# Performance work log

Hardware: AMD Instinct MI355X
Metric: run time of the kernel (lower is better)

The kernel has to match this reference:

```python
import jax, jax.numpy as jnp
import numpy as np

B, N, D = 4, 4096, 512
E = 4 * D            # expanded_dim = 2048
TAIL = E // 2        # tail_dim = 1024
HALF = TAIL // 2     # mt_half = 512
HEAD = E - TAIL      # head_dim = 1024
EPS_RMS = 1e-6
EPS_NORM = 1e-12


def setup_inputs() -> dict:
    key = jax.random.key(0)
    k = jax.random.split(key, 6)
    x = jax.random.normal(k[0], (B, N, D), dtype=jnp.float32)
    g = jnp.ones((D,), dtype=jnp.float32)                                   # RMSNorm gain
    W1 = jax.random.normal(k[1], (D, E), dtype=jnp.float32) * 0.02          # Enricher linear
    b1 = jnp.zeros((E,), dtype=jnp.float32)
    V = jax.random.normal(k[2], (N, N), dtype=jnp.float32) * 0.02           # learned positional matrix slice
    bias = jnp.zeros((HALF,), dtype=jnp.float32)                            # contextualizer bias
    Wf = jax.random.normal(k[3], (HEAD + HALF, D), dtype=jnp.float32) * 0.02  # Fuser linear (no bias)
    return {"x": x, "g": g, "W1": W1, "b1": b1, "V": V, "bias": bias, "Wf": Wf}


def reference(x, g, W1, b1, V, bias, Wf):
    # RMSNorm
    xn = x * jax.lax.rsqrt(jnp.mean(jnp.square(x), axis=-1, keepdims=True) + EPS_RMS) * g
    # Enricher: relu(linear)^2
    enriched = jnp.square(jax.nn.relu(xn @ W1 + b1))                        # [B, N, E]
    head = enriched[..., :HEAD]                                             # [B, N, HEAD]
    tail = enriched[..., HEAD:]                                             # [B, N, TAIL]
    # Contextualizer
    x_left = tail[..., :HALF]
    x_right = tail[..., HALF:]
    nrm = jnp.sqrt(jnp.sum(jnp.square(x_right), axis=-1, keepdims=True))
    xr_n = x_right / jnp.maximum(nrm, EPS_NORM)                             # F.normalize, p=2
    cos = jnp.einsum('bnd,bmd->bnm', xr_n, xr_n)                            # [B, N, N] cosine sim
    weighted = V[None, :, :] * cos                                          # elementwise learned V
    ctx = jnp.einsum('bnm,bmd->bnd', weighted, xr_n)                        # chunked-path bmm uses x_right_norm
    ctx = jax.nn.sigmoid(ctx + bias)
    gated = x_left * ctx                                                    # [B, N, HALF]
    # Fuser + residual
    out = jnp.concatenate([head, gated], axis=-1) @ Wf                      # [B, N, D]
    return x + out
```

## Files before the change

### kernel.cpp

```cpp
#include <hip/hip_runtime.h>
#include <stdint.h>

typedef unsigned short u16;
typedef unsigned long long u64;
typedef __attribute__((ext_vector_type(8))) short bf16x8;
typedef __attribute__((ext_vector_type(4))) float f32x4;
typedef __attribute__((ext_vector_type(16))) float f32x16;
typedef __attribute__((ext_vector_type(4))) unsigned int u32x4;
typedef __attribute__((ext_vector_type(4))) unsigned short u16x4;

#define DEV static __device__ __forceinline__

DEV u16 f2bf(float f){
  unsigned u = __builtin_bit_cast(unsigned, f);
  u += 0x7fffu + ((u >> 16) & 1u);
  return (u16)(u >> 16);
}
DEV float bf2f(u16 v){
  unsigned u = ((unsigned)v) << 16;
  return __builtin_bit_cast(float, u);
}

DEV void async_lds16(const void* g, void* l){
  __builtin_amdgcn_global_load_lds(
      (const __attribute__((address_space(1))) unsigned int*)g,
      (__attribute__((address_space(3))) unsigned int*)l, 16, 0, 0);
}

DEV f32x4 mfma16(bf16x8 a, bf16x8 b, f32x4 c){
  return __builtin_amdgcn_mfma_f32_16x16x32_bf16(a, b, c, 0, 0, 0);
}
DEV f32x16 mfma32(bf16x8 a, bf16x8 b, f32x16 c){
  return __builtin_amdgcn_mfma_f32_32x32x16_bf16(a, b, c, 0, 0, 0);
}

__global__ __launch_bounds__(64) void k_rms(const float* __restrict__ x,
                                            const float* __restrict__ g,
                                            u16* __restrict__ xn){
  const int row = blockIdx.x;
  const int l = threadIdx.x;
  const float* xr = x + (size_t)row * 512 + l * 8;
  f32x4 a = *(const f32x4*)xr;
  f32x4 c = *(const f32x4*)(xr + 4);
  float s = a[0]*a[0]+a[1]*a[1]+a[2]*a[2]+a[3]*a[3]
          + c[0]*c[0]+c[1]*c[1]+c[2]*c[2]+c[3]*c[3];
  #pragma unroll
  for (int off = 32; off >= 1; off >>= 1) s += __shfl_xor(s, off);
  float sc = rsqrtf(s * (1.f/512.f) + 1e-6f);
  f32x4 g0 = *(const f32x4*)&g[l*8];
  f32x4 g1 = *(const f32x4*)&g[l*8+4];
  u32x4 o;
  o[0] = (unsigned)f2bf(a[0]*sc*g0[0]) | ((unsigned)f2bf(a[1]*sc*g0[1]) << 16);
  o[1] = (unsigned)f2bf(a[2]*sc*g0[2]) | ((unsigned)f2bf(a[3]*sc*g0[3]) << 16);
  o[2] = (unsigned)f2bf(c[0]*sc*g1[0]) | ((unsigned)f2bf(c[1]*sc*g1[1]) << 16);
  o[3] = (unsigned)f2bf(c[2]*sc*g1[2]) | ((unsigned)f2bf(c[3]*sc*g1[3]) << 16);
  *(u32x4*)&xn[(size_t)row*512 + l*8] = o;
}

__global__ __launch_bounds__(64) void k_norm(const float* __restrict__ xr_in,
                                             u16* __restrict__ xrn){
  const int row = blockIdx.x;
  const int l = threadIdx.x;
  const float* xr = xr_in + (size_t)row * 512 + l * 8;
  f32x4 a = *(const f32x4*)xr;
  f32x4 c = *(const f32x4*)(xr + 4);
  float s = a[0]*a[0]+a[1]*a[1]+a[2]*a[2]+a[3]*a[3]
          + c[0]*c[0]+c[1]*c[1]+c[2]*c[2]+c[3]*c[3];
  #pragma unroll
  for (int off = 32; off >= 1; off >>= 1) s += __shfl_xor(s, off);
  float sc = 1.f / fmaxf(sqrtf(s), 1e-12f);
  u32x4 o;
  o[0] = (unsigned)f2bf(a[0]*sc) | ((unsigned)f2bf(a[1]*sc) << 16);
  o[1] = (unsigned)f2bf(a[2]*sc) | ((unsigned)f2bf(a[3]*sc) << 16);
  o[2] = (unsigned)f2bf(c[0]*sc) | ((unsigned)f2bf(c[1]*sc) << 16);
  o[3] = (unsigned)f2bf(c[2]*sc) | ((unsigned)f2bf(c[3]*sc) << 16);
  *(u32x4*)&xrn[(size_t)row*512 + l*8] = o;
}

__global__ __launch_bounds__(256) void k_tr32(const float* __restrict__ in,
                                              u16* __restrict__ out, int R, int C){
  __shared__ float tile[32][33];
  const int t = threadIdx.x;
  const int r = t >> 3;
  const int c4 = (t & 7) << 2;
  const int r0 = blockIdx.y << 5, c0 = blockIdx.x << 5;
  f32x4 v = *(const f32x4*)&in[(size_t)(r0 + r) * C + c0 + c4];
  tile[r][c4+0]=v[0]; tile[r][c4+1]=v[1]; tile[r][c4+2]=v[2]; tile[r][c4+3]=v[3];
  __syncthreads();
  u64 o =
      (u64)f2bf(tile[c4+0][r])
    | ((u64)f2bf(tile[c4+1][r]) << 16)
    | ((u64)f2bf(tile[c4+2][r]) << 32)
    | ((u64)f2bf(tile[c4+3][r]) << 48);
  *(u64*)&out[(size_t)(c0 + r) * R + r0 + c4] = o;
}

__global__ __launch_bounds__(256) void k_trb(const u16* __restrict__ in,
                                             u16* __restrict__ out, int R, int C){
  __shared__ u16 tile[32][40];
  const int t = threadIdx.x;
  const int r = t >> 3;
  const int c4 = (t & 7) << 2;
  const size_t bb = (size_t)blockIdx.z * R * C;
  const int r0 = blockIdx.y << 5, c0 = blockIdx.x << 5;
  u64 v = *(const u64*)&in[bb + (size_t)(r0 + r)*C + c0 + c4];
  tile[r][c4+0]=(u16)v; tile[r][c4+1]=(u16)(v>>16);
  tile[r][c4+2]=(u16)(v>>32); tile[r][c4+3]=(u16)(v>>48);
  __syncthreads();
  u64 o =
      (u64)tile[c4+0][r]
    | ((u64)tile[c4+1][r] << 16)
    | ((u64)tile[c4+2][r] << 32)
    | ((u64)tile[c4+3][r] << 48);
  *(u64*)&out[bb + (size_t)(c0 + r) * R + r0 + c4] = o;
}

__global__ __launch_bounds__(256) void k_gemm1(const u16* __restrict__ A,
                                               const u16* __restrict__ Bt,
                                               const float* __restrict__ b1,
                                               u16* __restrict__ head,
                                               float* __restrict__ xleft,
                                               float* __restrict__ xright){
  __shared__ u16 As[2][128*32];
  __shared__ u16 Bs[2][128*32];
  const int t = threadIdx.x;
  const int l = t & 63;
  const int w = t >> 6;
  const int wr = w >> 1, wc = w & 1;
  const int m0 = blockIdx.x << 7;
  const int n0 = blockIdx.y << 7;
  const int ra = t >> 2;
  const int kb = (t & 3) << 3;
  const int lr = l & 15, lh = l >> 4;
  f32x4 acc[4][4];
  #pragma unroll
  for (int i=0;i<4;i++)
    #pragma unroll
    for (int j=0;j<4;j++)
      #pragma unroll
      for (int r=0;r<4;r++) acc[i][j][r] = 0.f;

  async_lds16(A  + (size_t)(m0 + ra)*512      + kb, &As[0][t*8]);
  async_lds16(A  + (size_t)(m0 + 64 + ra)*512 + kb, &As[0][2048 + t*8]);
  async_lds16(Bt + (size_t)(n0 + ra)*512      + kb, &Bs[0][t*8]);
  async_lds16(Bt + (size_t)(n0 + 64 + ra)*512 + kb, &Bs[0][2048 + t*8]);
  __syncthreads();

  int cur = 0;
  for (int k0 = 0; k0 < 512; k0 += 32){
    if (k0 + 32 < 512){
      const int kn = k0 + 32;
      const int nb = cur ^ 1;
      async_lds16(A  + (size_t)(m0 + ra)*512      + kn + kb, &As[nb][t*8]);
      async_lds16(A  + (size_t)(m0 + 64 + ra)*512 + kn + kb, &As[nb][2048 + t*8]);
      async_lds16(Bt + (size_t)(n0 + ra)*512      + kn + kb, &Bs[nb][t*8]);
      async_lds16(Bt + (size_t)(n0 + 64 + ra)*512 + kn + kb, &Bs[nb][2048 + t*8]);
    }
    bf16x8 af[4], bfr[4];
    #pragma unroll
    for (int i=0;i<4;i++){
      af[i]  = *(const bf16x8*)&As[cur][(wr*64 + i*16 + lr)*32 + lh*8];
      bfr[i] = *(const bf16x8*)&Bs[cur][(wc*64 + i*16 + lr)*32 + lh*8];
    }
    #pragma unroll
    for (int i=0;i<4;i++)
      #pragma unroll
      for (int j=0;j<4;j++)
        acc[i][j] = mfma16(af[i], bfr[j], acc[i][j]);
    __syncthreads();
    cur ^= 1;
  }
  #pragma unroll
  for (int i=0;i<4;i++){
    #pragma unroll
    for (int j=0;j<4;j++){
      int c = n0 + wc*64 + j*16 + lr;
      float bb = b1[c];
      #pragma unroll
      for (int r=0;r<4;r++){
        int m = m0 + wr*64 + i*16 + lh*4 + r;
        float v = acc[i][j][r] + bb;
        v = v > 0.f ? v*v : 0.f;
        if (c < 1024)      head[(size_t)m*1024 + c] = f2bf(v);
        else if (c < 1536) xleft[(size_t)m*512 + (c - 1024)] = v;
        else               xright[(size_t)m*512 + (c - 1536)] = v;
      }
    }
  }
}

__global__ __launch_bounds__(256) void k_gemm3(const u16* __restrict__ head,
                                               const u16* __restrict__ gated,
                                               const u16* __restrict__ Wft,
                                               const float* __restrict__ x,
                                               float* __restrict__ out){
  __shared__ u16 As[2][128*32];
  __shared__ u16 Bs[2][128*32];
  const int t = threadIdx.x;
  const int l = t & 63;
  const int w = t >> 6;
  const int wr = w >> 1, wc = w & 1;
  const int m0 = blockIdx.x << 7;
  const int n0 = blockIdx.y << 7;
  const int ra = t >> 2;
  const int kb = (t & 3) << 3;
  const int lr = l & 15, lh = l >> 4;
  f32x4 acc[4][4];
  #pragma unroll
  for (int i=0;i<4;i++)
    #pragma unroll
    for (int j=0;j<4;j++)
      #pragma unroll
      for (int r=0;r<4;r++) acc[i][j][r] = 0.f;

  auto stage = [&](int nb, int k0){
    const u16* sa; size_t lda; int kk;
    if (k0 < 1024){ sa = head;  lda = 1024; kk = k0; }
    else          { sa = gated; lda = 512;  kk = k0 - 1024; }
    async_lds16(sa + (size_t)(m0 + ra)*lda      + kk + kb, &As[nb][t*8]);
    async_lds16(sa + (size_t)(m0 + 64 + ra)*lda + kk + kb, &As[nb][2048 + t*8]);
    async_lds16(Wft + (size_t)(n0 + ra)*1536      + k0 + kb, &Bs[nb][t*8]);
    async_lds16(Wft + (size_t)(n0 + 64 + ra)*1536 + k0 + kb, &Bs[nb][2048 + t*8]);
  };
  stage(0, 0);
  __syncthreads();

  int cur = 0;
  for (int k0 = 0; k0 < 1536; k0 += 32){
    if (k0 + 32 < 1536) stage(cur ^ 1, k0 + 32);
    bf16x8 af[4], bfr[4];
    #pragma unroll
    for (int i=0;i<4;i++){
      af[i]  = *(const bf16x8*)&As[cur][(wr*64 + i*16 + lr)*32 + lh*8];
      bfr[i] = *(const bf16x8*)&Bs[cur][(wc*64 + i*16 + lr)*32 + lh*8];
    }
    #pragma unroll
    for (int i=0;i<4;i++)
      #pragma unroll
      for (int j=0;j<4;j++)
        acc[i][j] = mfma16(af[i], bfr[j], acc[i][j]);
    __syncthreads();
    cur ^= 1;
  }
  #pragma unroll
  for (int i=0;i<4;i++){
    #pragma unroll
    for (int j=0;j<4;j++){
      int c = n0 + wc*64 + j*16 + lr;
      #pragma unroll
      for (int r=0;r<4;r++){
        int m = m0 + wr*64 + i*16 + lh*4 + r;
        size_t gi = (size_t)m*512 + c;
        out[gi] = x[gi] + acc[i][j][r];
      }
    }
  }
}

__global__ __launch_bounds__(512, 2) void k_attn(const u16* __restrict__ xrn,
                                                 const u16* __restrict__ xrT,
                                                 const float* __restrict__ V,
                                                 const float* __restrict__ bias,
                                                 const float* __restrict__ xleft,
                                                 u16* __restrict__ gated){
  __shared__ char smem[154624];
  char* km = smem;
  char* tt = smem + 65536;
  char* ps = smem + 131072;
  char* pb = smem + 149504;
  const int t = threadIdx.x;
  const int l = t & 63, w = t >> 6;
  const int wr = w >> 2, ks = w & 3, wc = (w >> 1) & 1, kq2 = w & 1;
  const int lo = l & 31, hi = l >> 5;
  const int bid = blockIdx.x;
  const int b  = (bid & 7) >> 1;
  const int n0 = ((((bid >> 3) << 1) | (bid & 1))) << 6;
  const u16* xb  = xrn + (size_t)b * (4096*512);
  const u16* xTb = xrT + (size_t)b * (512*4096);

  bf16x8 areg[8];
  {
    const u16* apt = xb + (size_t)(n0 + wr*32 + lo)*512 + ks*128 + hi*8;
    #pragma unroll
    for (int kq = 0; kq < 8; ++kq) areg[kq] = *(const bf16x8*)(apt + kq*16);
  }
  f32x16 acc[8];
  #pragma unroll
  for (int i = 0; i < 8; ++i)
    #pragma unroll
    for (int j = 0; j < 16; ++j) acc[i][j] = 0.f;

  const int prf = t >> 3;
  const int pc4 = (t & 7) << 2;
  const int wrr = prf >> 5, prr = prf & 31;

  #pragma unroll
  for (int c = 0; c < 4; ++c){
    int off = (c*512 + t)*16;
    int row = off >> 10, colb = off & 1023;
    async_lds16(xb + (size_t)row*512 + ((colb ^ ((row&7)<<4)) >> 1), km + off);
    int dr = off >> 6, cb2 = off & 63;
    async_lds16(xTb + (size_t)dr*4096 + ((cb2 ^ ((dr&6)<<3)) >> 1), tt + off);
  }
  __syncthreads();

  int cur = 0;
  for (int it = 0; it < 128; ++it){
    const int m0 = it << 5;
    f32x4 vf = *(const f32x4*)&V[(size_t)(n0 + prf)*4096 + m0 + pc4];
    if (it < 127){
      const int m1 = m0 + 32;
      const int nb = (cur ^ 1) * 32768;
      #pragma unroll
      for (int c = 0; c < 4; ++c){
        int off = (c*512 + t)*16;
        int row = off >> 10, colb = off & 1023;
        async_lds16(xb + (size_t)(m1 + row)*512 + ((colb ^ ((row&7)<<4)) >> 1),
                    km + nb + off);
        int dr = off >> 6, cb2 = off & 63;
        async_lds16(xTb + (size_t)dr*4096 + m1 + ((cb2 ^ ((dr&6)<<3)) >> 1),
                    tt + nb + off);
      }
    }
    f32x16 S0, S1;
    #pragma unroll
    for (int j = 0; j < 16; ++j){ S0[j] = 0.f; S1[j] = 0.f; }
    {
      const char* kbp = km + cur*32768 + lo*1024;
      const int swk = (lo & 7) << 4;
      #pragma unroll
      for (int kq = 0; kq < 8; kq += 2){
        bf16x8 b0 = *(const bf16x8*)(kbp + ((ks*256 + kq*32 + hi*16) ^ swk));
        bf16x8 b1 = *(const bf16x8*)(kbp + ((ks*256 + (kq+1)*32 + hi*16) ^ swk));
        S0 = mfma32(areg[kq],   b0, S0);
        S1 = mfma32(areg[kq+1], b1, S1);
      }
    }
    {
      char* pw = ps + ((wr*4 + ks)*32)*72 + lo*2;
      #pragma unroll
      for (int rg = 0; rg < 16; ++rg){
        int prow = (rg & 3) + 8*(rg >> 2) + 4*hi;
        *(u16*)(pw + prow*72) = f2bf(S0[rg] + S1[rg]);
      }
    }
    asm volatile("s_waitcnt lgkmcnt(0)" ::: "memory");
    __builtin_amdgcn_s_barrier();
    __builtin_amdgcn_sched_barrier(0);
    {
      float s0=0.f, s1=0.f, s2=0.f, s3=0.f;
      #pragma unroll
      for (int k2 = 0; k2 < 4; ++k2){
        u16x4 pv = *(const u16x4*)(ps + (((wrr*4 + k2)*32 + prr)*36 + pc4)*2);
        s0 += bf2f(pv[0]); s1 += bf2f(pv[1]); s2 += bf2f(pv[2]); s3 += bf2f(pv[3]);
      }
      u64 po = (u64)f2bf(s0 * vf[0])
             | ((u64)f2bf(s1 * vf[1]) << 16)
             | ((u64)f2bf(s2 * vf[2]) << 32)
             | ((u64)f2bf(s3 * vf[3]) << 48);
      *(u64*)(pb + (prf*40 + pc4)*2) = po;
    }
    asm volatile("s_waitcnt lgkmcnt(0)" ::: "memory");
    __builtin_amdgcn_s_barrier();
    __builtin_amdgcn_sched_barrier(0);
    {
      bf16x8 pa = *(const bf16x8*)(pb + (wr*32 + lo)*80 + kq2*32 + hi*16);
      const char* tb = tt + cur*32768;
      #pragma unroll
      for (int ds = 0; ds < 8; ++ds){
        int drow = wc*256 + ds*32 + lo;
        bf16x8 bfr = *(const bf16x8*)(tb + drow*64 +
                       ((kq2*32 + hi*16) ^ ((drow & 6) << 3)));
        acc[ds] = mfma32(pa, bfr, acc[ds]);
      }
    }
    __syncthreads();
    cur ^= 1;
  }

  float* red = (float*)smem;
  const int rbase = (wr*2 + wc) * 8192;
  if (kq2 == 1){
    #pragma unroll
    for (int ds = 0; ds < 8; ++ds)
      #pragma unroll
      for (int rg = 0; rg < 16; ++rg)
        red[rbase + (ds*16 + rg)*64 + l] = acc[ds][rg];
  }
  __syncthreads();
  if (kq2 == 0){
    #pragma unroll
    for (int ds = 0; ds < 8; ++ds){
      const int d = wc*256 + ds*32 + lo;
      const float bs = bias[d];
      #pragma unroll
      for (int rg = 0; rg < 16; ++rg){
        int row = n0 + wr*32 + (rg & 3) + 8*(rg >> 2) + 4*hi;
        float v = acc[ds][rg] + red[rbase + (ds*16 + rg)*64 + l] + bs;
        v = 1.f / (1.f + __expf(-v));
        size_t gi = (size_t)(b*4096 + row)*512 + d;
        gated[gi] = f2bf(xleft[gi] * v);
      }
    }
  }
}

extern "C" void kernel_launch(void* const* d_in, const int* in_sizes, int n_in,
                              void* d_out, int out_size, void* d_ws, size_t ws_size,
                              hipStream_t stream){
  const float* x    = (const float*)d_in[0];
  const float* g    = (const float*)d_in[1];
  const float* W1   = (const float*)d_in[2];
  const float* b1   = (const float*)d_in[3];
  const float* V    = (const float*)d_in[4];
  const float* bias = (const float*)d_in[5];
  const float* Wf   = (const float*)d_in[6];
  float* out = (float*)d_out;

  char* ws = (char*)d_ws;
  const size_t MB = 1024u*1024u;
  u16*   xn     = (u16*)  (ws + 0*MB);
  u16*   W1t    = (u16*)  (ws + 16*MB);
  u16*   Wft    = (u16*)  (ws + 18*MB);
  u16*   head   = (u16*)  (ws + 20*MB);
  float* xleft  = (float*)(ws + 52*MB);
  float* xright = (float*)(ws + 84*MB);
  u16*   gated  = (u16*)  (ws + 84*MB);
  u16*   xrn    = (u16*)  (ws + 116*MB);
  u16*   xrT    = (u16*)  (ws + 132*MB);

  k_rms  <<<dim3(16384),      dim3(64),  0, stream>>>(x, g, xn);
  k_tr32 <<<dim3(64, 16),     dim3(256), 0, stream>>>(W1, W1t, 512, 2048);
  k_tr32 <<<dim3(16, 48),     dim3(256), 0, stream>>>(Wf, Wft, 1536, 512);
  k_gemm1<<<dim3(128, 16),    dim3(256), 0, stream>>>(xn, W1t, b1, head, xleft, xright);
  k_norm <<<dim3(16384),      dim3(64),  0, stream>>>(xright, xrn);
  k_trb  <<<dim3(16, 128, 4), dim3(256), 0, stream>>>(xrn, xrT, 4096, 512);
  k_attn <<<dim3(256),        dim3(512), 0, stream>>>(xrn, xrT, V, bias, xleft, gated);
  k_gemm3<<<dim3(128, 4),     dim3(256), 0, stream>>>(head, gated, Wft, x, out);
}
```

Before: 385.0 us.

## Warp-specialize attention kernel into S-producer and PV-consumer wave groups

Splits the eight waves into four that compute the cosine-similarity tile S and four that apply V and accumulate P·X, with the consumer lagging one iteration behind through a double-buffered S tile in LDS. This removes one barrier per iteration and the final cross-wave reduction of the accumulators, since each consumer wave now covers the full K range of its tile. The cost is a deeper software pipeline, extra LDS, twice the A-fragment registers in producer waves, and possible imbalance between the two wave groups.

```diff
diff --git a/kernel.cpp b/kernel.cpp
--- a/kernel.cpp
+++ b/kernel.cpp
@@ -20,6 +20,7 @@
   unsigned u = ((unsigned)v) << 16;
   return __builtin_bit_cast(float, u);
 }
+DEV float bitf(unsigned u){ return __builtin_bit_cast(float, u); }
 
 DEV void async_lds16(const void* g, void* l){
   __builtin_amdgcn_global_load_lds(
@@ -263,140 +264,142 @@
                                                  const float* __restrict__ bias,
                                                  const float* __restrict__ xleft,
                                                  u16* __restrict__ gated){
-  __shared__ char smem[154624];
+  __shared__ char smem[156672];
   char* km = smem;
   char* tt = smem + 65536;
   char* ps = smem + 131072;
-  char* pb = smem + 149504;
+  char* pb = smem + 151552;
   const int t = threadIdx.x;
   const int l = t & 63, w = t >> 6;
-  const int wr = w >> 2, ks = w & 3, wc = (w >> 1) & 1, kq2 = w & 1;
   const int lo = l & 31, hi = l >> 5;
+  const bool isS = (w < 4);
+  const int wr  = (w >> 1) & 1;
+  const int sub = w & 1;
   const int bid = blockIdx.x;
   const int b  = (bid & 7) >> 1;
   const int n0 = ((((bid >> 3) << 1) | (bid & 1))) << 6;
   const u16* xb  = xrn + (size_t)b * (4096*512);
   const u16* xTb = xrT + (size_t)b * (512*4096);
 
-  bf16x8 areg[8];
-  {
-    const u16* apt = xb + (size_t)(n0 + wr*32 + lo)*512 + ks*128 + hi*8;
-    #pragma unroll
-    for (int kq = 0; kq < 8; ++kq) areg[kq] = *(const bf16x8*)(apt + kq*16);
+  bf16x8 areg[16];
+  if (isS){
+    const u16* apt = xb + (size_t)(n0 + wr*32 + lo)*512 + sub*256 + hi*8;
+    #pragma unroll
+    for (int kq = 0; kq < 16; ++kq) areg[kq] = *(const bf16x8*)(apt + kq*16);
   }
   f32x16 acc[8];
   #pragma unroll
   for (int i = 0; i < 8; ++i)
     #pragma unroll
     for (int j = 0; j < 16; ++j) acc[i][j] = 0.f;
-
-  const int prf = t >> 3;
-  const int pc4 = (t & 7) << 2;
-  const int wrr = prf >> 5, prr = prf & 31;
 
   #pragma unroll
   for (int c = 0; c < 4; ++c){
     int off = (c*512 + t)*16;
     int row = off >> 10, colb = off & 1023;
     async_lds16(xb + (size_t)row*512 + ((colb ^ ((row&7)<<4)) >> 1), km + off);
-    int dr = off >> 6, cb2 = off & 63;
-    async_lds16(xTb + (size_t)dr*4096 + ((cb2 ^ ((dr&6)<<3)) >> 1), tt + off);
-  }
-  __syncthreads();
-
-  int cur = 0;
-  for (int it = 0; it < 128; ++it){
-    const int m0 = it << 5;
-    f32x4 vf = *(const f32x4*)&V[(size_t)(n0 + prf)*4096 + m0 + pc4];
+  }
+
+  f32x4 v0n = {0,0,0,0}, v1n = {0,0,0,0}, v0c = {0,0,0,0}, v1c = {0,0,0,0};
+
+  for (int it = 0; it <= 128; ++it){
+    __syncthreads();
     if (it < 127){
-      const int m1 = m0 + 32;
-      const int nb = (cur ^ 1) * 32768;
+      const int m1 = (it + 1) << 5;
+      const int nb = ((it + 1) & 1) * 32768;
       #pragma unroll
       for (int c = 0; c < 4; ++c){
         int off = (c*512 + t)*16;
         int row = off >> 10, colb = off & 1023;
         async_lds16(xb + (size_t)(m1 + row)*512 + ((colb ^ ((row&7)<<4)) >> 1),
                     km + nb + off);
+      }
+    }
+    if (it < 128){
+      const int mt = it << 5;
+      const int nb = (it & 1) * 32768;
+      #pragma unroll
+      for (int c = 0; c < 4; ++c){
+        int off = (c*512 + t)*16;
         int dr = off >> 6, cb2 = off & 63;
-        async_lds16(xTb + (size_t)dr*4096 + m1 + ((cb2 ^ ((dr&6)<<3)) >> 1),
+        async_lds16(xTb + (size_t)dr*4096 + mt + ((cb2 ^ ((dr&6)<<3)) >> 1),
                     tt + nb + off);
       }
     }
-    f32x16 S0, S1;
-    #pragma unroll
-    for (int j = 0; j < 16; ++j){ S0[j] = 0.f; S1[j] = 0.f; }
-    {
-      const char* kbp = km + cur*32768 + lo*1024;
-      const int swk = (lo & 7) << 4;
-      #pragma unroll
-      for (int kq = 0; kq < 8; kq += 2){
-        bf16x8 b0 = *(const bf16x8*)(kbp + ((ks*256 + kq*32 + hi*16) ^ swk));
-        bf16x8 b1 = *(const bf16x8*)(kbp + ((ks*256 + (kq+1)*32 + hi*16) ^ swk));
-        S0 = mfma32(areg[kq],   b0, S0);
-        S1 = mfma32(areg[kq+1], b1, S1);
-      }
-    }
-    {
-      char* pw = ps + ((wr*4 + ks)*32)*72 + lo*2;
-      #pragma unroll
-      for (int rg = 0; rg < 16; ++rg){
-        int prow = (rg & 3) + 8*(rg >> 2) + 4*hi;
-        *(u16*)(pw + prow*72) = f2bf(S0[rg] + S1[rg]);
+    if (isS){
+      if (it < 128){
+        f32x16 S0, S1;
+        #pragma unroll
+        for (int j = 0; j < 16; ++j){ S0[j] = 0.f; S1[j] = 0.f; }
+        const char* kbp = km + (it & 1)*32768 + lo*1024;
+        const int swk = (lo & 7) << 4;
+        #pragma unroll
+        for (int kq = 0; kq < 16; kq += 2){
+          bf16x8 b0 = *(const bf16x8*)(kbp + ((sub*512 + kq*32 + hi*16) ^ swk));
+          bf16x8 b1 = *(const bf16x8*)(kbp + ((sub*512 + (kq+1)*32 + hi*16) ^ swk));
+          S0 = mfma32(areg[kq],   b0, S0);
+          S1 = mfma32(areg[kq+1], b1, S1);
+        }
+        char* pw = ps + (it & 1)*10240 + (wr*2 + sub)*2560 + lo*2;
+        #pragma unroll
+        for (int rg = 0; rg < 16; ++rg){
+          int prow = (rg & 3) + 8*(rg >> 2) + 4*hi;
+          *(u16*)(pw + prow*80) = f2bf(S0[rg] + S1[rg]);
+        }
+      }
+    } else {
+      if (it < 128){
+        const float* vp = V + (size_t)(n0 + wr*32 + lo)*4096 + (it << 5)
+                        + sub*16 + hi*8;
+        v0n = *(const f32x4*)vp;
+        v1n = *(const f32x4*)(vp + 4);
+      }
+      if (it > 0){
+        const char* pr = ps + ((it - 1) & 1)*10240 + (wr*2)*2560 + lo*80
+                       + sub*32 + hi*16;
+        u32x4 qa = *(const u32x4*)pr;
+        u32x4 qb = *(const u32x4*)(pr + 2560);
+        u32x4 pk;
+        #pragma unroll
+        for (int e = 0; e < 4; ++e){
+          float se = bitf(qa[e] << 16) + bitf(qb[e] << 16);
+          float so = bitf(qa[e] & 0xffff0000u) + bitf(qb[e] & 0xffff0000u);
+          float ve = (e < 2) ? v0c[e*2]     : v1c[(e - 2)*2];
+          float vo = (e < 2) ? v0c[e*2 + 1] : v1c[(e - 2)*2 + 1];
+          pk[e] = (unsigned)f2bf(se * ve) | ((unsigned)f2bf(so * vo) << 16);
+        }
+        *(u32x4*)(pb + (wr*32 + lo)*80 + sub*32 + hi*16) = pk;
       }
     }
     asm volatile("s_waitcnt lgkmcnt(0)" ::: "memory");
     __builtin_amdgcn_s_barrier();
     __builtin_amdgcn_sched_barrier(0);
-    {
-      float s0=0.f, s1=0.f, s2=0.f, s3=0.f;
-      #pragma unroll
-      for (int k2 = 0; k2 < 4; ++k2){
-        u16x4 pv = *(const u16x4*)(ps + (((wrr*4 + k2)*32 + prr)*36 + pc4)*2);
-        s0 += bf2f(pv[0]); s1 += bf2f(pv[1]); s2 += bf2f(pv[2]); s3 += bf2f(pv[3]);
-      }
-      u64 po = (u64)f2bf(s0 * vf[0])
-             | ((u64)f2bf(s1 * vf[1]) << 16)
-             | ((u64)f2bf(s2 * vf[2]) << 32)
-             | ((u64)f2bf(s3 * vf[3]) << 48);
-      *(u64*)(pb + (prf*40 + pc4)*2) = po;
-    }
-    asm volatile("s_waitcnt lgkmcnt(0)" ::: "memory");
-    __builtin_amdgcn_s_barrier();
-    __builtin_amdgcn_sched_barrier(0);
-    {
-      bf16x8 pa = *(const bf16x8*)(pb + (wr*32 + lo)*80 + kq2*32 + hi*16);
-      const char* tb = tt + cur*32768;
-      #pragma unroll
-      for (int ds = 0; ds < 8; ++ds){
-        int drow = wc*256 + ds*32 + lo;
-        bf16x8 bfr = *(const bf16x8*)(tb + drow*64 +
-                       ((kq2*32 + hi*16) ^ ((drow & 6) << 3)));
-        acc[ds] = mfma32(pa, bfr, acc[ds]);
-      }
-    }
-    __syncthreads();
-    cur ^= 1;
-  }
-
-  float* red = (float*)smem;
-  const int rbase = (wr*2 + wc) * 8192;
-  if (kq2 == 1){
-    #pragma unroll
-    for (int ds = 0; ds < 8; ++ds)
-      #pragma unroll
-      for (int rg = 0; rg < 16; ++rg)
-        red[rbase + (ds*16 + rg)*64 + l] = acc[ds][rg];
-  }
-  __syncthreads();
-  if (kq2 == 0){
+    if (!isS && it > 0){
+      const char* tb = tt + ((it - 1) & 1)*32768;
+      #pragma unroll
+      for (int kq2 = 0; kq2 < 2; ++kq2){
+        bf16x8 pa = *(const bf16x8*)(pb + (wr*32 + lo)*80 + kq2*32 + hi*16);
+        #pragma unroll
+        for (int ds = 0; ds < 8; ++ds){
+          int drow = sub*256 + ds*32 + lo;
+          bf16x8 bfr = *(const bf16x8*)(tb + drow*64 +
+                         ((kq2*32 + hi*16) ^ ((drow & 6) << 3)));
+          acc[ds] = mfma32(pa, bfr, acc[ds]);
+        }
+      }
+    }
+    v0c = v0n; v1c = v1n;
+  }
+
+  if (!isS){
     #pragma unroll
     for (int ds = 0; ds < 8; ++ds){
-      const int d = wc*256 + ds*32 + lo;
+      const int d = sub*256 + ds*32 + lo;
       const float bs = bias[d];
       #pragma unroll
       for (int rg = 0; rg < 16; ++rg){
         int row = n0 + wr*32 + (rg & 3) + 8*(rg >> 2) + 4*hi;
-        float v = acc[ds][rg] + red[rbase + (ds*16 + rg)*64 + l] + bs;
+        float v = acc[ds][rg] + bs;
         v = 1.f / (1.f + __expf(-v));
         size_t gi = (size_t)(b*4096 + row)*512 + d;
         gated[gi] = f2bf(xleft[gi] * v);
```

After: 679.2 us. 1.76x slower.

## Split fused attention kernel into separate S-GEMM and PV-GEMM with materialized P

Applied to the files above, without the earlier changes.

Replaces the fused cosine-attention kernel with two plain tiled GEMM kernels: one computes the cosine matrix times V and writes a bf16 P matrix to global memory, the other multiplies P by the transposed normalized keys and applies the sigmoid gate. The workspace layout is reorganized so all batches' P fit when the workspace is large enough, with a per-batch loop as fallback. This trades the fused kernel's LDS round-trips and barriers for simpler, higher-occupancy GEMMs at the cost of writing and reading a 32 MB-per-batch intermediate.

```diff
diff --git a/kernel.cpp b/kernel.cpp
--- a/kernel.cpp
+++ b/kernel.cpp
@@ -5,9 +5,7 @@
 typedef unsigned long long u64;
 typedef __attribute__((ext_vector_type(8))) short bf16x8;
 typedef __attribute__((ext_vector_type(4))) float f32x4;
-typedef __attribute__((ext_vector_type(16))) float f32x16;
 typedef __attribute__((ext_vector_type(4))) unsigned int u32x4;
-typedef __attribute__((ext_vector_type(4))) unsigned short u16x4;
 
 #define DEV static __device__ __forceinline__
 
@@ -16,10 +14,6 @@
   u += 0x7fffu + ((u >> 16) & 1u);
   return (u16)(u >> 16);
 }
-DEV float bf2f(u16 v){
-  unsigned u = ((unsigned)v) << 16;
-  return __builtin_bit_cast(float, u);
-}
 
 DEV void async_lds16(const void* g, void* l){
   __builtin_amdgcn_global_load_lds(
@@ -29,9 +23,6 @@
 
 DEV f32x4 mfma16(bf16x8 a, bf16x8 b, f32x4 c){
   return __builtin_amdgcn_mfma_f32_16x16x32_bf16(a, b, c, 0, 0, 0);
-}
-DEV f32x16 mfma32(bf16x8 a, bf16x8 b, f32x16 c){
-  return __builtin_amdgcn_mfma_f32_32x32x16_bf16(a, b, c, 0, 0, 0);
 }
 
 __global__ __launch_bounds__(64) void k_rms(const float* __restrict__ x,
@@ -257,148 +248,143 @@
   }
 }
 
-__global__ __launch_bounds__(512, 2) void k_attn(const u16* __restrict__ xrn,
-                                                 const u16* __restrict__ xrT,
-                                                 const float* __restrict__ V,
-                                                 const float* __restrict__ bias,
-                                                 const float* __restrict__ xleft,
-                                                 u16* __restrict__ gated){
-  __shared__ char smem[154624];
-  char* km = smem;
-  char* tt = smem + 65536;
-  char* ps = smem + 131072;
-  char* pb = smem + 149504;
-  const int t = threadIdx.x;
-  const int l = t & 63, w = t >> 6;
-  const int wr = w >> 2, ks = w & 3, wc = (w >> 1) & 1, kq2 = w & 1;
-  const int lo = l & 31, hi = l >> 5;
-  const int bid = blockIdx.x;
-  const int b  = (bid & 7) >> 1;
-  const int n0 = ((((bid >> 3) << 1) | (bid & 1))) << 6;
-  const u16* xb  = xrn + (size_t)b * (4096*512);
-  const u16* xTb = xrT + (size_t)b * (512*4096);
-
-  bf16x8 areg[8];
-  {
-    const u16* apt = xb + (size_t)(n0 + wr*32 + lo)*512 + ks*128 + hi*8;
-    #pragma unroll
-    for (int kq = 0; kq < 8; ++kq) areg[kq] = *(const bf16x8*)(apt + kq*16);
-  }
-  f32x16 acc[8];
-  #pragma unroll
-  for (int i = 0; i < 8; ++i)
-    #pragma unroll
-    for (int j = 0; j < 16; ++j) acc[i][j] = 0.f;
-
-  const int prf = t >> 3;
-  const int pc4 = (t & 7) << 2;
-  const int wrr = prf >> 5, prr = prf & 31;
-
-  #pragma unroll
-  for (int c = 0; c < 4; ++c){
-    int off = (c*512 + t)*16;
-    int row = off >> 10, colb = off & 1023;
-    async_lds16(xb + (size_t)row*512 + ((colb ^ ((row&7)<<4)) >> 1), km + off);
-    int dr = off >> 6, cb2 = off & 63;
-    async_lds16(xTb + (size_t)dr*4096 + ((cb2 ^ ((dr&6)<<3)) >> 1), tt + off);
-  }
+__global__ __launch_bounds__(256) void k_sgemm(const u16* __restrict__ xrn,
+                                               const float* __restrict__ V,
+                                               u16* __restrict__ P,
+                                               size_t pstride, int b0){
+  __shared__ u16 As[2][128*32];
+  __shared__ u16 Bs[2][128*32];
+  const int t = threadIdx.x;
+  const int l = t & 63;
+  const int w = t >> 6;
+  const int wr = w >> 1, wc = w & 1;
+  const int m0 = blockIdx.x << 7;
+  const int n0 = blockIdx.y << 7;
+  const int b  = b0 + blockIdx.z;
+  const u16* xb = xrn + (size_t)b * (4096*512);
+  u16* Pb = P + (size_t)blockIdx.z * pstride;
+  const int ra = t >> 2;
+  const int kb = (t & 3) << 3;
+  const int lr = l & 15, lh = l >> 4;
+  f32x4 acc[4][4];
+  #pragma unroll
+  for (int i=0;i<4;i++)
+    #pragma unroll
+    for (int j=0;j<4;j++)
+      #pragma unroll
+      for (int r=0;r<4;r++) acc[i][j][r] = 0.f;
+
+  async_lds16(xb + (size_t)(n0 + ra)*512      + kb, &As[0][t*8]);
+  async_lds16(xb + (size_t)(n0 + 64 + ra)*512 + kb, &As[0][2048 + t*8]);
+  async_lds16(xb + (size_t)(m0 + ra)*512      + kb, &Bs[0][t*8]);
+  async_lds16(xb + (size_t)(m0 + 64 + ra)*512 + kb, &Bs[0][2048 + t*8]);
   __syncthreads();
 
   int cur = 0;
-  for (int it = 0; it < 128; ++it){
-    const int m0 = it << 5;
-    f32x4 vf = *(const f32x4*)&V[(size_t)(n0 + prf)*4096 + m0 + pc4];
-    if (it < 127){
-      const int m1 = m0 + 32;
-      const int nb = (cur ^ 1) * 32768;
-      #pragma unroll
-      for (int c = 0; c < 4; ++c){
-        int off = (c*512 + t)*16;
-        int row = off >> 10, colb = off & 1023;
-        async_lds16(xb + (size_t)(m1 + row)*512 + ((colb ^ ((row&7)<<4)) >> 1),
-                    km + nb + off);
-        int dr = off >> 6, cb2 = off & 63;
-        async_lds16(xTb + (size_t)dr*4096 + m1 + ((cb2 ^ ((dr&6)<<3)) >> 1),
-                    tt + nb + off);
-      }
-    }
-    f32x16 S0, S1;
-    #pragma unroll
-    for (int j = 0; j < 16; ++j){ S0[j] = 0.f; S1[j] = 0.f; }
-    {
-      const char* kbp = km + cur*32768 + lo*1024;
-      const int swk = (lo & 7) << 4;
-      #pragma unroll
-      for (int kq = 0; kq < 8; kq += 2){
-        bf16x8 b0 = *(const bf16x8*)(kbp + ((ks*256 + kq*32 + hi*16) ^ swk));
-        bf16x8 b1 = *(const bf16x8*)(kbp + ((ks*256 + (kq+1)*32 + hi*16) ^ swk));
-        S0 = mfma32(areg[kq],   b0, S0);
-        S1 = mfma32(areg[kq+1], b1, S1);
-      }
-    }
-    {
-      char* pw = ps + ((wr*4 + ks)*32)*72 + lo*2;
-      #pragma unroll
-      for (int rg = 0; rg < 16; ++rg){
-        int prow = (rg & 3) + 8*(rg >> 2) + 4*hi;
-        *(u16*)(pw + prow*72) = f2bf(S0[rg] + S1[rg]);
-      }
-    }
-    asm volatile("s_waitcnt lgkmcnt(0)" ::: "memory");
-    __builtin_amdgcn_s_barrier();
-    __builtin_amdgcn_sched_barrier(0);
-    {
-      float s0=0.f, s1=0.f, s2=0.f, s3=0.f;
-      #pragma unroll
-      for (int k2 = 0; k2 < 4; ++k2){
-        u16x4 pv = *(const u16x4*)(ps + (((wrr*4 + k2)*32 + prr)*36 + pc4)*2);
-        s0 += bf2f(pv[0]); s1 += bf2f(pv[1]); s2 += bf2f(pv[2]); s3 += bf2f(pv[3]);
-      }
-      u64 po = (u64)f2bf(s0 * vf[0])
-             | ((u64)f2bf(s1 * vf[1]) << 16)
-             | ((u64)f2bf(s2 * vf[2]) << 32)
-             | ((u64)f2bf(s3 * vf[3]) << 48);
-      *(u64*)(pb + (prf*40 + pc4)*2) = po;
-    }
-    asm volatile("s_waitcnt lgkmcnt(0)" ::: "memory");
-    __builtin_amdgcn_s_barrier();
-    __builtin_amdgcn_sched_barrier(0);
-    {
-      bf16x8 pa = *(const bf16x8*)(pb + (wr*32 + lo)*80 + kq2*32 + hi*16);
-      const char* tb = tt + cur*32768;
-      #pragma unroll
-      for (int ds = 0; ds < 8; ++ds){
-        int drow = wc*256 + ds*32 + lo;
-        bf16x8 bfr = *(const bf16x8*)(tb + drow*64 +
-                       ((kq2*32 + hi*16) ^ ((drow & 6) << 3)));
-        acc[ds] = mfma32(pa, bfr, acc[ds]);
-      }
-    }
+  for (int k0 = 0; k0 < 512; k0 += 32){
+    if (k0 + 32 < 512){
+      const int kn = k0 + 32;
+      const int nb = cur ^ 1;
+      async_lds16(xb + (size_t)(n0 + ra)*512      + kn + kb, &As[nb][t*8]);
+      async_lds16(xb + (size_t)(n0 + 64 + ra)*512 + kn + kb, &As[nb][2048 + t*8]);
+      async_lds16(xb + (size_t)(m0 + ra)*512      + kn + kb, &Bs[nb][t*8]);
+      async_lds16(xb + (size_t)(m0 + 64 + ra)*512 + kn + kb, &Bs[nb][2048 + t*8]);
+    }
+    bf16x8 af[4], bfr[4];
+    #pragma unroll
+    for (int i=0;i<4;i++){
+      af[i]  = *(const bf16x8*)&As[cur][(wr*64 + i*16 + lr)*32 + lh*8];
+      bfr[i] = *(const bf16x8*)&Bs[cur][(wc*64 + i*16 + lr)*32 + lh*8];
+    }
+    #pragma unroll
+    for (int i=0;i<4;i++)
+      #pragma unroll
+      for (int j=0;j<4;j++)
+        acc[i][j] = mfma16(af[i], bfr[j], acc[i][j]);
     __syncthreads();
     cur ^= 1;
   }
-
-  float* red = (float*)smem;
-  const int rbase = (wr*2 + wc) * 8192;
-  if (kq2 == 1){
-    #pragma unroll
-    for (int ds = 0; ds < 8; ++ds)
-      #pragma unroll
-      for (int rg = 0; rg < 16; ++rg)
-        red[rbase + (ds*16 + rg)*64 + l] = acc[ds][rg];
-  }
-  __syncthreads();
-  if (kq2 == 0){
-    #pragma unroll
-    for (int ds = 0; ds < 8; ++ds){
-      const int d = wc*256 + ds*32 + lo;
-      const float bs = bias[d];
-      #pragma unroll
-      for (int rg = 0; rg < 16; ++rg){
-        int row = n0 + wr*32 + (rg & 3) + 8*(rg >> 2) + 4*hi;
-        float v = acc[ds][rg] + red[rbase + (ds*16 + rg)*64 + l] + bs;
+  #pragma unroll
+  for (int i=0;i<4;i++){
+    #pragma unroll
+    for (int j=0;j<4;j++){
+      int col = m0 + wc*64 + j*16 + lr;
+      #pragma unroll
+      for (int r=0;r<4;r++){
+        int row = n0 + wr*64 + i*16 + lh*4 + r;
+        float vv = V[(size_t)row*4096 + col];
+        Pb[(size_t)row*4096 + col] = f2bf(acc[i][j][r] * vv);
+      }
+    }
+  }
+}
+
+__global__ __launch_bounds__(256) void k_pvgemm(const u16* __restrict__ P,
+                                                size_t pstride,
+                                                const u16* __restrict__ xrT,
+                                                const float* __restrict__ xleft,
+                                                const float* __restrict__ bias,
+                                                u16* __restrict__ gated, int b0){
+  __shared__ u16 As[2][64*32];
+  __shared__ u16 Bs[2][128*32];
+  const int t = threadIdx.x;
+  const int l = t & 63;
+  const int w = t >> 6;
+  const int wr = w >> 1, wc = w & 1;
+  const int n0 = blockIdx.x << 6;
+  const int d0 = blockIdx.y << 7;
+  const int b  = b0 + blockIdx.z;
+  const u16* Pb  = P + (size_t)blockIdx.z * pstride;
+  const u16* xTb = xrT + (size_t)b * (512*4096);
+  const int ra = t >> 2;
+  const int kb = (t & 3) << 3;
+  const int lr = l & 15, lh = l >> 4;
+  f32x4 acc[2][4];
+  #pragma unroll
+  for (int i=0;i<2;i++)
+    #pragma unroll
+    for (int j=0;j<4;j++)
+      #pragma unroll
+      for (int r=0;r<4;r++) acc[i][j][r] = 0.f;
+
+  auto stage = [&](int nb, int k0){
+    async_lds16(Pb  + (size_t)(n0 + ra)*4096       + k0 + kb, &As[nb][t*8]);
+    async_lds16(xTb + (size_t)(d0 + ra)*4096       + k0 + kb, &Bs[nb][t*8]);
+    async_lds16(xTb + (size_t)(d0 + 64 + ra)*4096  + k0 + kb, &Bs[nb][2048 + t*8]);
+  };
+  stage(0, 0);
+  __syncthreads();
+
+  int cur = 0;
+  for (int k0 = 0; k0 < 4096; k0 += 32){
+    if (k0 + 32 < 4096) stage(cur ^ 1, k0 + 32);
+    bf16x8 af[2], bfr[4];
+    #pragma unroll
+    for (int i=0;i<2;i++)
+      af[i]  = *(const bf16x8*)&As[cur][(wr*32 + i*16 + lr)*32 + lh*8];
+    #pragma unroll
+    for (int j=0;j<4;j++)
+      bfr[j] = *(const bf16x8*)&Bs[cur][(wc*64 + j*16 + lr)*32 + lh*8];
+    #pragma unroll
+    for (int i=0;i<2;i++)
+      #pragma unroll
+      for (int j=0;j<4;j++)
+        acc[i][j] = mfma16(af[i], bfr[j], acc[i][j]);
+    __syncthreads();
+    cur ^= 1;
+  }
+  #pragma unroll
+  for (int i=0;i<2;i++){
+    #pragma unroll
+    for (int j=0;j<4;j++){
+      int d = d0 + wc*64 + j*16 + lr;
+      float bs = bias[d];
+      #pragma unroll
+      for (int r=0;r<4;r++){
+        int n = n0 + wr*32 + i*16 + lh*4 + r;
+        float v = acc[i][j][r] + bs;
         v = 1.f / (1.f + __expf(-v));
-        size_t gi = (size_t)(b*4096 + row)*512 + d;
+        size_t gi = (size_t)(b*4096 + n)*512 + d;
         gated[gi] = f2bf(xleft[gi] * v);
       }
     }
@@ -418,16 +404,35 @@
   float* out = (float*)d_out;
 
   char* ws = (char*)d_ws;
-  const size_t MB = 1024u*1024u;
-  u16*   xn     = (u16*)  (ws + 0*MB);
-  u16*   W1t    = (u16*)  (ws + 16*MB);
-  u16*   Wft    = (u16*)  (ws + 18*MB);
-  u16*   head   = (u16*)  (ws + 20*MB);
-  float* xleft  = (float*)(ws + 52*MB);
-  float* xright = (float*)(ws + 84*MB);
-  u16*   gated  = (u16*)  (ws + 84*MB);
-  u16*   xrn    = (u16*)  (ws + 116*MB);
-  u16*   xrT    = (u16*)  (ws + 132*MB);
+  const size_t MiB = 1024u*1024u;
+  const size_t PSTR = (size_t)4096 * 4096;
+  const bool full = ws_size >= 244*MiB;
+
+  u16 *xn, *W1t, *Wft, *head, *gated, *xrn, *xrT, *P;
+  float *xleft, *xright;
+  if (full){
+    P      = (u16*)  (ws + 0*MiB);
+    xn     = (u16*)  (ws + 0*MiB);
+    W1t    = (u16*)  (ws + 16*MiB);
+    xright = (float*)(ws + 18*MiB);
+    head   = (u16*)  (ws + 128*MiB);
+    xleft  = (float*)(ws + 160*MiB);
+    xrn    = (u16*)  (ws + 192*MiB);
+    xrT    = (u16*)  (ws + 208*MiB);
+    Wft    = (u16*)  (ws + 224*MiB);
+    gated  = (u16*)  (ws + 226*MiB);
+  } else {
+    xn     = (u16*)  (ws + 0*MiB);
+    W1t    = (u16*)  (ws + 16*MiB);
+    Wft    = (u16*)  (ws + 18*MiB);
+    head   = (u16*)  (ws + 20*MiB);
+    xleft  = (float*)(ws + 52*MiB);
+    xright = (float*)(ws + 84*MiB);
+    P      = (u16*)  (ws + 84*MiB);
+    xrn    = (u16*)  (ws + 116*MiB);
+    xrT    = (u16*)  (ws + 132*MiB);
+    gated  = (u16*)  (ws + 148*MiB);
+  }
 
   k_rms  <<<dim3(16384),      dim3(64),  0, stream>>>(x, g, xn);
   k_tr32 <<<dim3(64, 16),     dim3(256), 0, stream>>>(W1, W1t, 512, 2048);
@@ -435,6 +440,16 @@
   k_gemm1<<<dim3(128, 16),    dim3(256), 0, stream>>>(xn, W1t, b1, head, xleft, xright);
   k_norm <<<dim3(16384),      dim3(64),  0, stream>>>(xright, xrn);
   k_trb  <<<dim3(16, 128, 4), dim3(256), 0, stream>>>(xrn, xrT, 4096, 512);
-  k_attn <<<dim3(256),        dim3(512), 0, stream>>>(xrn, xrT, V, bias, xleft, gated);
+
+  if (full){
+    k_sgemm <<<dim3(32, 32, 4), dim3(256), 0, stream>>>(xrn, V, P, PSTR, 0);
+    k_pvgemm<<<dim3(64, 4, 4),  dim3(256), 0, stream>>>(P, PSTR, xrT, xleft, bias, gated, 0);
+  } else {
+    for (int b = 0; b < 4; ++b){
+      k_sgemm <<<dim3(32, 32, 1), dim3(256), 0, stream>>>(xrn, V, P, 0, b);
+      k_pvgemm<<<dim3(64, 4, 1),  dim3(256), 0, stream>>>(P, 0, xrT, xleft, bias, gated, b);
+    }
+  }
+
   k_gemm3<<<dim3(128, 4),     dim3(256), 0, stream>>>(head, gated, Wft, x, out);
 }
```

Result: slower. 472.6 us (+22.8%).
